# Kernel optimization log

Hardware: AMD Instinct MI355X
Metric: run time of the kernel (lower is better)

## Reference

```python
import jax, jax.numpy as jnp
import numpy as np

V, T, K, L, D = 256, 256, 36, 32, 1024
TAU = 0.05
MODE = 0
NEG_INF = -jnp.inf


def setup_inputs() -> dict:
    key = jax.random.key(0)
    k1, k2 = jax.random.split(key)
    imgs = jax.random.normal(k1, (V, K, D), dtype=jnp.float32)
    caps = jax.random.normal(k2, (T, L, D), dtype=jnp.float32)
    # Full lengths: the original module writes -inf into sim and 0 into w at
    # padded positions, so padding would produce -inf*0 = NaN in the output.
    img_lens = jnp.full((V,), K, dtype=jnp.int32)
    cap_lens = jnp.full((T,), L, dtype=jnp.int32)
    return {"imgs": imgs, "caps": caps, "img_lens": img_lens, "cap_lens": cap_lens}


def _l2norm(x):
    return x / jnp.maximum(jnp.linalg.norm(x, axis=-1, keepdims=True), 1e-12)


def reference(imgs, caps, img_lens, cap_lens):
    # masks: [V,K], [T,L]
    img_mask = (jnp.arange(K)[None, :] < img_lens[:, None]).astype(imgs.dtype)
    cap_mask = (jnp.arange(L)[None, :] < cap_lens[:, None]).astype(caps.dtype)
    # AvePool: masked mean over valid tokens, then L2-normalize
    img_glo = _l2norm((imgs * img_mask[:, :, None]).sum(1) / img_lens[:, None].astype(imgs.dtype))
    cap_glo = _l2norm((caps * cap_mask[:, :, None]).sum(1) / cap_lens[:, None].astype(caps.dtype))
    # ds: [V,T,K], et: [V,T,L]  (computed as in the original; note the original
    # forward overwrites w with the masked sim, so ds/et/softmax do not affect
    # the returned value — we keep only the live dataflow here)
    ds = jnp.einsum('vkd,td->vtk', imgs, cap_glo)
    et = jnp.einsum('tld,vd->vtl', caps, img_glo)
    del ds, et  # dead in the original (w is reassigned to masked sim)
    # sim: [V,T,K,L]
    sim = jnp.einsum('vkd,tld->vtkl', imgs, caps)
    sim_mask = img_mask[:, None, :, None] * cap_mask[None, :, None, :]  # [V,T,K,L]
    valid = sim_mask != 0
    sim = jnp.where(valid, sim, NEG_INF)
    # final w in the original is sim.masked_fill(sim_mask == 0, 0)
    w = jnp.where(valid, sim, 0.0)
    return jnp.einsum('vtkl,vtkl->vt', sim, w)
```

## Files before the change

kernel.cpp:

```cpp
#include <hip/hip_runtime.h>

#define V_N 256
#define T_N 256
#define K_N 36
#define L_N 32
#define D_N 1024
#define MROWS (V_N * K_N)
#define NROWS (T_N * L_N)
#define BM 256
#define BN 256
#define BK 64
#define KSTEPS (D_N / BK)
#define NBM (MROWS / BM)
#define NBN (NROWS / BN)
#define NWG (NBM * NBN)

typedef __attribute__((ext_vector_type(8))) short bf16x8;
typedef __attribute__((ext_vector_type(4))) float f32x4;

__device__ __forceinline__ ushort f2bf(float x) {
  union { float f; unsigned int u; } c; c.f = x;
  unsigned int r = c.u + 0x7FFFu + ((c.u >> 16) & 1u);
  return (ushort)(r >> 16);
}

__global__ void cvt_cast(const float* __restrict__ imgs, const float* __restrict__ caps,
                         ushort* __restrict__ aws, ushort* __restrict__ bws) {
  const int AQ = MROWS * (D_N / 4);
  const int BQ = NROWS * (D_N / 4);
  const int total = AQ + BQ;
  for (int q = blockIdx.x * blockDim.x + threadIdx.x; q < total;
       q += gridDim.x * blockDim.x) {
    float4 f;
    ushort4* dst;
    if (q < AQ) {
      f = reinterpret_cast<const float4*>(imgs)[q];
      dst = reinterpret_cast<ushort4*>(aws) + q;
    } else {
      f = reinterpret_cast<const float4*>(caps)[q - AQ];
      dst = reinterpret_cast<ushort4*>(bws) + (q - AQ);
    }
    ushort4 u; u.x = f2bf(f.x); u.y = f2bf(f.y); u.z = f2bf(f.z); u.w = f2bf(f.w);
    *dst = u;
  }
}

__global__ __launch_bounds__(512, 2) void gemm2(
    const ushort* __restrict__ aws, const ushort* __restrict__ bws,
    float* __restrict__ out) {
  __shared__ ushort lds[2 * 2 * BM * BK];

  int orig = (int)blockIdx.x;
  int wg = (orig & 7) * (NWG / 8) + (orig >> 3);
  const int bm = wg / NBN;
  const int bn = wg % NBN;
  const int row0 = bm * BM;
  const int col0 = bn * BN;

  const int tid  = (int)threadIdx.x;
  const int lane = tid & 63;
  const int wid  = tid >> 6;
  const int wr   = wid >> 2;
  const int wc   = wid & 3;

  auto stageA = [&](int kt) {
    ushort* bufA = lds + (kt & 1) * (2 * BM * BK);
#pragma unroll
    for (int it = 0; it < 4; ++it) {
      int q = it * 512 + tid;
      int r = q >> 3;
      int sw = ((q & 7) << 4) ^ ((r & 7) << 4);
      const ushort* ga = aws + (size_t)(row0 + r) * D_N + kt * BK + (sw >> 1);
      __builtin_amdgcn_global_load_lds(
          (const __attribute__((address_space(1))) void*)ga,
          (__attribute__((address_space(3))) void*)(bufA + q * 8), 16, 0, 0);
    }
  };
  auto stageB = [&](int kt) {
    ushort* bufB = lds + (kt & 1) * (2 * BM * BK) + BM * BK;
#pragma unroll
    for (int it = 0; it < 4; ++it) {
      int q = it * 512 + tid;
      int r = q >> 3;
      int sw = ((q & 7) << 4) ^ ((r & 7) << 4);
      const ushort* gb = bws + (size_t)(col0 + r) * D_N + kt * BK + (sw >> 1);
      __builtin_amdgcn_global_load_lds(
          (const __attribute__((address_space(1))) void*)gb,
          (__attribute__((address_space(3))) void*)(bufB + q * 8), 16, 0, 0);
    }
  };

  f32x4 acc[8][4];
#pragma unroll
  for (int m = 0; m < 8; ++m)
#pragma unroll
    for (int n = 0; n < 4; ++n) acc[m][n] = (f32x4){0.f, 0.f, 0.f, 0.f};

  const int arow = wr * 128 + (lane & 15);
  const int brow = wc * 64 + (lane & 15);
  const int kb   = (lane >> 4) << 4;
  const int swz  = (lane & 7) << 4;

  auto tile = [&](int t, int do_stage) {
    const ushort* bufA = lds + (t & 1) * (2 * BM * BK);
    const ushort* bufB = bufA + BM * BK;
    const int sw0 = (kb) ^ swz;
    const int sw1 = (64 + kb) ^ swz;

    bf16x8 a0[8], a1[8], b0[4], b1[4];
#pragma unroll
    for (int m = 0; m < 4; ++m)
      a0[m] = *reinterpret_cast<const bf16x8*>(bufA + (arow + m * 16) * BK + (sw0 >> 1));
#pragma unroll
    for (int n = 0; n < 4; ++n)
      b0[n] = *reinterpret_cast<const bf16x8*>(bufB + (brow + n * 16) * BK + (sw0 >> 1));
#pragma unroll
    for (int m = 4; m < 8; ++m)
      a0[m] = *reinterpret_cast<const bf16x8*>(bufA + (arow + m * 16) * BK + (sw0 >> 1));
#pragma unroll
    for (int m = 0; m < 4; ++m)
      a1[m] = *reinterpret_cast<const bf16x8*>(bufA + (arow + m * 16) * BK + (sw1 >> 1));
#pragma unroll
    for (int n = 0; n < 4; ++n)
      b1[n] = *reinterpret_cast<const bf16x8*>(bufB + (brow + n * 16) * BK + (sw1 >> 1));
#pragma unroll
    for (int m = 4; m < 8; ++m)
      a1[m] = *reinterpret_cast<const bf16x8*>(bufA + (arow + m * 16) * BK + (sw1 >> 1));

    __builtin_amdgcn_s_setprio(1);
#pragma unroll
    for (int m = 0; m < 4; ++m)
#pragma unroll
      for (int n = 0; n < 4; ++n)
        acc[m][n] = __builtin_amdgcn_mfma_f32_16x16x32_bf16(a0[m], b0[n], acc[m][n], 0, 0, 0);
    __builtin_amdgcn_s_setprio(0);
    __builtin_amdgcn_s_setprio(1);
#pragma unroll
    for (int m = 4; m < 8; ++m)
#pragma unroll
      for (int n = 0; n < 4; ++n)
        acc[m][n] = __builtin_amdgcn_mfma_f32_16x16x32_bf16(a0[m], b0[n], acc[m][n], 0, 0, 0);
    __builtin_amdgcn_s_setprio(0);
    __builtin_amdgcn_s_setprio(1);
#pragma unroll
    for (int m = 0; m < 4; ++m)
#pragma unroll
      for (int n = 0; n < 4; ++n)
        acc[m][n] = __builtin_amdgcn_mfma_f32_16x16x32_bf16(a1[m], b1[n], acc[m][n], 0, 0, 0);
    __builtin_amdgcn_s_setprio(0);

    asm volatile("s_waitcnt lgkmcnt(0)" ::: "memory");
    __builtin_amdgcn_sched_barrier(0);
    __builtin_amdgcn_s_barrier();
    __builtin_amdgcn_sched_barrier(0);

    if (do_stage) { stageA(t + 2); stageB(t + 2); }

    __builtin_amdgcn_s_setprio(1);
#pragma unroll
    for (int m = 4; m < 8; ++m)
#pragma unroll
      for (int n = 0; n < 4; ++n)
        acc[m][n] = __builtin_amdgcn_mfma_f32_16x16x32_bf16(a1[m], b1[n], acc[m][n], 0, 0, 0);
    __builtin_amdgcn_s_setprio(0);
  };

  stageA(0); stageB(0);
  stageA(1); stageB(1);
  asm volatile("s_waitcnt vmcnt(8)" ::: "memory");
  __builtin_amdgcn_sched_barrier(0);
  __builtin_amdgcn_s_barrier();
  __builtin_amdgcn_sched_barrier(0);

  for (int t = 0; t < KSTEPS - 2; ++t) {
    tile(t, 1);
    asm volatile("s_waitcnt vmcnt(8)" ::: "memory");
    __builtin_amdgcn_sched_barrier(0);
    __builtin_amdgcn_s_barrier();
    __builtin_amdgcn_sched_barrier(0);
  }
  tile(KSTEPS - 2, 0);
  asm volatile("s_waitcnt vmcnt(0)" ::: "memory");
  __builtin_amdgcn_sched_barrier(0);
  __builtin_amdgcn_s_barrier();
  __builtin_amdgcn_sched_barrier(0);
  tile(KSTEPS - 1, 0);

#pragma unroll
  for (int m = 0; m < 8; ++m) {
    int grow = row0 + wr * 128 + m * 16;
    int v0 = grow / K_N;
    int b = (v0 + 1) * K_N;
    int rb = grow + ((lane >> 4) << 2);
#pragma unroll
    for (int np = 0; np < 2; ++np) {
      float s0 = 0.f, s1 = 0.f;
#pragma unroll
      for (int nn = 0; nn < 2; ++nn) {
        f32x4 a4 = acc[m][np * 2 + nn];
#pragma unroll
        for (int rg = 0; rg < 4; ++rg) {
          float x = a4[rg];
          float x2 = x * x;
          if (rb + rg < b) s0 += x2; else s1 += x2;
        }
      }
#pragma unroll
      for (int off = 32; off > 0; off >>= 1) {
        s0 += __shfl_xor(s0, off, 64);
        s1 += __shfl_xor(s1, off, 64);
      }
      if (lane == 0) {
        int tcol = (col0 + wc * 64 + np * 32) >> 5;
        atomicAdd(out + v0 * T_N + tcol, s0);
        if (grow + 16 > b) atomicAdd(out + (v0 + 1) * T_N + tcol, s1);
      }
    }
  }
}

__global__ __launch_bounds__(256) void gemm_fb(
    const float* __restrict__ imgs, const float* __restrict__ caps,
    float* __restrict__ out) {
  __shared__ ushort lds[128 * 64 + 128 * 64];
  ushort* ldsA = lds;
  ushort* ldsB = lds + 128 * 64;
  const int NBMf = MROWS / 128, NBNf = NROWS / 128;
  int orig = (int)blockIdx.x;
  int xcd = orig & 7;
  int idx = orig >> 3;
  int bm = xcd * (NBMf / 8) + (idx / NBNf);
  int bn = idx % NBNf;
  const int row0 = bm * 128, col0 = bn * 128;
  const int tid = (int)threadIdx.x, lane = tid & 63, wid = tid >> 6;
  const int wr = wid >> 1, wc = wid & 1;
  f32x4 acc[4][4];
#pragma unroll
  for (int i = 0; i < 4; ++i)
#pragma unroll
    for (int j = 0; j < 4; ++j) acc[i][j] = (f32x4){0.f, 0.f, 0.f, 0.f};
  for (int kt = 0; kt < KSTEPS; ++kt) {
#pragma unroll
    for (int it = 0; it < 4; ++it) {
      int q = it * 256 + tid;
      int r = q >> 3;
      int sw = ((q & 7) << 4) ^ ((r & 7) << 4);
      const float4* src = reinterpret_cast<const float4*>(
          imgs + (size_t)(row0 + r) * D_N + kt * BK + (sw >> 1));
      float4 f0 = src[0], f1 = src[1];
      union { ushort u[8]; int4 v4; } pk;
      pk.u[0] = f2bf(f0.x); pk.u[1] = f2bf(f0.y); pk.u[2] = f2bf(f0.z); pk.u[3] = f2bf(f0.w);
      pk.u[4] = f2bf(f1.x); pk.u[5] = f2bf(f1.y); pk.u[6] = f2bf(f1.z); pk.u[7] = f2bf(f1.w);
      *reinterpret_cast<int4*>(ldsA + q * 8) = pk.v4;
    }
#pragma unroll
    for (int it = 0; it < 4; ++it) {
      int q = it * 256 + tid;
      int r = q >> 3;
      int sw = ((q & 7) << 4) ^ ((r & 7) << 4);
      const float4* src = reinterpret_cast<const float4*>(
          caps + (size_t)(col0 + r) * D_N + kt * BK + (sw >> 1));
      float4 f0 = src[0], f1 = src[1];
      union { ushort u[8]; int4 v4; } pk;
      pk.u[0] = f2bf(f0.x); pk.u[1] = f2bf(f0.y); pk.u[2] = f2bf(f0.z); pk.u[3] = f2bf(f0.w);
      pk.u[4] = f2bf(f1.x); pk.u[5] = f2bf(f1.y); pk.u[6] = f2bf(f1.z); pk.u[7] = f2bf(f1.w);
      *reinterpret_cast<int4*>(ldsB + q * 8) = pk.v4;
    }
    __syncthreads();
#pragma unroll
    for (int ks = 0; ks < 2; ++ks) {
      bf16x8 afr[4], bfr[4];
#pragma unroll
      for (int i = 0; i < 4; ++i) {
        int r = wr * 64 + i * 16 + (lane & 15);
        int sw = (ks * 64 + (((lane >> 4) << 4))) ^ ((r & 7) << 4);
        afr[i] = *reinterpret_cast<const bf16x8*>(ldsA + r * BK + (sw >> 1));
      }
#pragma unroll
      for (int j = 0; j < 4; ++j) {
        int r = wc * 64 + j * 16 + (lane & 15);
        int sw = (ks * 64 + (((lane >> 4) << 4))) ^ ((r & 7) << 4);
        bfr[j] = *reinterpret_cast<const bf16x8*>(ldsB + r * BK + (sw >> 1));
      }
#pragma unroll
      for (int i = 0; i < 4; ++i)
#pragma unroll
        for (int j = 0; j < 4; ++j)
          acc[i][j] = __builtin_amdgcn_mfma_f32_16x16x32_bf16(afr[i], bfr[j], acc[i][j], 0, 0, 0);
    }
    __syncthreads();
  }
#pragma unroll
  for (int i = 0; i < 4; ++i) {
#pragma unroll
    for (int j = 0; j < 4; ++j) {
      f32x4 a4 = acc[i][j];
      int grow = row0 + wr * 64 + i * 16;
      int gcol = col0 + wc * 64 + j * 16;
      int t = gcol >> 5;
      int v0 = grow / K_N;
      int b = (v0 + 1) * K_N;
      int rbase = grow + ((lane >> 4) << 2);
      float s0 = 0.f, s1 = 0.f;
#pragma unroll
      for (int rg = 0; rg < 4; ++rg) {
        float x = a4[rg];
        float x2 = x * x;
        if (rbase + rg < b) s0 += x2; else s1 += x2;
      }
#pragma unroll
      for (int off = 32; off > 0; off >>= 1) {
        s0 += __shfl_xor(s0, off, 64);
        s1 += __shfl_xor(s1, off, 64);
      }
      if (lane == 0) {
        atomicAdd(out + v0 * T_N + t, s0);
        if (b < grow + 16) atomicAdd(out + (v0 + 1) * T_N + t, s1);
      }
    }
  }
}

extern "C" void kernel_launch(void* const* d_in, const int* in_sizes, int n_in,
                              void* d_out, int out_size, void* d_ws, size_t ws_size,
                              hipStream_t stream) {
  const float* imgs = (const float*)d_in[0];
  const float* caps = (const float*)d_in[1];
  float* out = (float*)d_out;

  hipMemsetAsync(d_out, 0, (size_t)V_N * T_N * sizeof(float), stream);

  const size_t need = (size_t)(MROWS + NROWS) * D_N * sizeof(ushort);

  if (ws_size >= need) {
    ushort* aws = (ushort*)d_ws;
    ushort* bws = aws + (size_t)MROWS * D_N;
    cvt_cast<<<2048, 256, 0, stream>>>(imgs, caps, aws, bws);
    gemm2<<<NWG, 512, 0, stream>>>(aws, bws, out);
  } else {
    const int nwg = (MROWS / 128) * (NROWS / 128);
    gemm_fb<<<nwg, 256, 0, stream>>>(imgs, caps, out);
  }
}
```

Baseline: 197.8 us.

## Split GEMM main loop into four quadrant phases with staggered LDS staging

```diff
diff --git a/kernel.cpp b/kernel.cpp
--- a/kernel.cpp
+++ b/kernel.cpp
@@ -17,6 +17,10 @@
 
 typedef __attribute__((ext_vector_type(8))) short bf16x8;
 typedef __attribute__((ext_vector_type(4))) float f32x4;
+
+#define SB0 __builtin_amdgcn_sched_barrier(0)
+#define BAR __builtin_amdgcn_s_barrier()
+#define LGK0 asm volatile("s_waitcnt lgkmcnt(0)" ::: "memory")
 
 __device__ __forceinline__ ushort f2bf(float x) {
   union { float f; unsigned int u; } c; c.f = x;
@@ -63,32 +67,36 @@
   const int wr   = wid >> 2;
   const int wc   = wid & 3;
 
-  auto stageA = [&](int kt) {
-    ushort* bufA = lds + (kt & 1) * (2 * BM * BK);
-#pragma unroll
-    for (int it = 0; it < 4; ++it) {
-      int q = it * 512 + tid;
-      int r = q >> 3;
-      int sw = ((q & 7) << 4) ^ ((r & 7) << 4);
-      const ushort* ga = aws + (size_t)(row0 + r) * D_N + kt * BK + (sw >> 1);
+  const int kb  = (lane >> 4) << 4;
+
+  auto stage_unit = [&](int kt, int kind) {
+    const int rb0 = (kind == 0) ? 0 : (kind == 1) ? 64 : (kind == 2) ? 0 : 128;
+    const int rb1 = (kind == 0) ? 128 : (kind == 1) ? 192 : (kind == 2) ? 64 : 192;
+    ushort* base = lds + (kt & 1) * (2 * BM * BK) + ((kind >= 2) ? BM * BK : 0);
+    const ushort* g = (kind >= 2) ? bws : aws;
+    const int g0 = (kind >= 2) ? col0 : row0;
+#pragma unroll
+    for (int j = 0; j < 2; ++j) {
+      int r = (j ? rb1 : rb0) + (tid >> 3);
+      int sw = ((tid & 7) << 4) ^ ((r & 7) << 4);
+      const ushort* src = g + (size_t)(g0 + r) * D_N + kt * BK + (sw >> 1);
       __builtin_amdgcn_global_load_lds(
-          (const __attribute__((address_space(1))) void*)ga,
-          (__attribute__((address_space(3))) void*)(bufA + q * 8), 16, 0, 0);
+          (const __attribute__((address_space(1))) void*)src,
+          (__attribute__((address_space(3))) void*)(base + r * BK + (tid & 7) * 8),
+          16, 0, 0);
     }
   };
-  auto stageB = [&](int kt) {
-    ushort* bufB = lds + (kt & 1) * (2 * BM * BK) + BM * BK;
-#pragma unroll
-    for (int it = 0; it < 4; ++it) {
-      int q = it * 512 + tid;
-      int r = q >> 3;
-      int sw = ((q & 7) << 4) ^ ((r & 7) << 4);
-      const ushort* gb = bws + (size_t)(col0 + r) * D_N + kt * BK + (sw >> 1);
-      __builtin_amdgcn_global_load_lds(
-          (const __attribute__((address_space(1))) void*)gb,
-          (__attribute__((address_space(3))) void*)(bufB + q * 8), 16, 0, 0);
-    }
+
+  auto rdA = [&](const ushort* bufA, int m, int ks) -> bf16x8 {
+    int r = wr * 128 + m * 16 + (lane & 15);
+    int sw = (ks * 64 + kb) ^ ((r & 7) << 4);
+    return *reinterpret_cast<const bf16x8*>(bufA + r * BK + (sw >> 1));
   };
+  auto rdB = [&](const ushort* bufB, int n, int ks) -> bf16x8 {
+    int r = wc * 64 + n * 16 + (lane & 15);
+    int sw = (ks * 64 + kb) ^ ((r & 7) << 4);
+    return *reinterpret_cast<const bf16x8*>(bufB + r * BK + (sw >> 1));
+  };
 
   f32x4 acc[8][4];
 #pragma unroll
@@ -96,95 +104,94 @@
 #pragma unroll
     for (int n = 0; n < 4; ++n) acc[m][n] = (f32x4){0.f, 0.f, 0.f, 0.f};
 
-  const int arow = wr * 128 + (lane & 15);
-  const int brow = wc * 64 + (lane & 15);
-  const int kb   = (lane >> 4) << 4;
-  const int swz  = (lane & 7) << 4;
-
-  auto tile = [&](int t, int do_stage) {
+  stage_unit(0, 0); stage_unit(0, 2); stage_unit(0, 3); stage_unit(0, 1);
+  stage_unit(1, 0); stage_unit(1, 2); stage_unit(1, 3);
+  asm volatile("s_waitcnt vmcnt(6)" ::: "memory");
+  SB0; BAR; SB0;
+
+  for (int t = 0; t < KSTEPS; ++t) {
     const ushort* bufA = lds + (t & 1) * (2 * BM * BK);
     const ushort* bufB = bufA + BM * BK;
-    const int sw0 = (kb) ^ swz;
-    const int sw1 = (64 + kb) ^ swz;
-
-    bf16x8 a0[8], a1[8], b0[4], b1[4];
-#pragma unroll
-    for (int m = 0; m < 4; ++m)
-      a0[m] = *reinterpret_cast<const bf16x8*>(bufA + (arow + m * 16) * BK + (sw0 >> 1));
-#pragma unroll
-    for (int n = 0; n < 4; ++n)
-      b0[n] = *reinterpret_cast<const bf16x8*>(bufB + (brow + n * 16) * BK + (sw0 >> 1));
-#pragma unroll
-    for (int m = 4; m < 8; ++m)
-      a0[m] = *reinterpret_cast<const bf16x8*>(bufA + (arow + m * 16) * BK + (sw0 >> 1));
-#pragma unroll
-    for (int m = 0; m < 4; ++m)
-      a1[m] = *reinterpret_cast<const bf16x8*>(bufA + (arow + m * 16) * BK + (sw1 >> 1));
-#pragma unroll
-    for (int n = 0; n < 4; ++n)
-      b1[n] = *reinterpret_cast<const bf16x8*>(bufB + (brow + n * 16) * BK + (sw1 >> 1));
-#pragma unroll
-    for (int m = 4; m < 8; ++m)
-      a1[m] = *reinterpret_cast<const bf16x8*>(bufA + (arow + m * 16) * BK + (sw1 >> 1));
-
+    bf16x8 aA[8], b01[4], b23[4];
+
+#pragma unroll
+    for (int m = 0; m < 4; ++m) { aA[m] = rdA(bufA, m, 0); aA[4 + m] = rdA(bufA, m, 1); }
+#pragma unroll
+    for (int n = 0; n < 2; ++n) { b01[n] = rdB(bufB, n, 0); b01[2 + n] = rdB(bufB, n, 1); }
+    if (t <= KSTEPS - 2) stage_unit(t + 1, 1);
+    SB0; BAR; LGK0; SB0;
     __builtin_amdgcn_s_setprio(1);
 #pragma unroll
     for (int m = 0; m < 4; ++m)
 #pragma unroll
-      for (int n = 0; n < 4; ++n)
-        acc[m][n] = __builtin_amdgcn_mfma_f32_16x16x32_bf16(a0[m], b0[n], acc[m][n], 0, 0, 0);
+      for (int n = 0; n < 2; ++n)
+        acc[m][n] = __builtin_amdgcn_mfma_f32_16x16x32_bf16(aA[m], b01[n], acc[m][n], 0, 0, 0);
+#pragma unroll
+    for (int m = 0; m < 4; ++m)
+#pragma unroll
+      for (int n = 0; n < 2; ++n)
+        acc[m][n] = __builtin_amdgcn_mfma_f32_16x16x32_bf16(aA[4 + m], b01[2 + n], acc[m][n], 0, 0, 0);
     __builtin_amdgcn_s_setprio(0);
+    SB0; BAR;
+
+#pragma unroll
+    for (int n = 0; n < 2; ++n) { b23[n] = rdB(bufB, 2 + n, 0); b23[2 + n] = rdB(bufB, 2 + n, 1); }
+    if (t <= KSTEPS - 3) stage_unit(t + 2, 0);
+    SB0; BAR; LGK0; SB0;
     __builtin_amdgcn_s_setprio(1);
 #pragma unroll
-    for (int m = 4; m < 8; ++m)
-#pragma unroll
-      for (int n = 0; n < 4; ++n)
-        acc[m][n] = __builtin_amdgcn_mfma_f32_16x16x32_bf16(a0[m], b0[n], acc[m][n], 0, 0, 0);
+    for (int m = 0; m < 4; ++m)
+#pragma unroll
+      for (int n = 0; n < 2; ++n)
+        acc[m][2 + n] = __builtin_amdgcn_mfma_f32_16x16x32_bf16(aA[m], b23[n], acc[m][2 + n], 0, 0, 0);
+#pragma unroll
+    for (int m = 0; m < 4; ++m)
+#pragma unroll
+      for (int n = 0; n < 2; ++n)
+        acc[m][2 + n] = __builtin_amdgcn_mfma_f32_16x16x32_bf16(aA[4 + m], b23[2 + n], acc[m][2 + n], 0, 0, 0);
     __builtin_amdgcn_s_setprio(0);
+    if (t <= KSTEPS - 3)      { asm volatile("s_waitcnt vmcnt(10)" ::: "memory"); }
+    else if (t == KSTEPS - 2) { asm volatile("s_waitcnt vmcnt(8)"  ::: "memory"); }
+    else                      { asm volatile("s_waitcnt vmcnt(0)"  ::: "memory"); }
+    SB0; BAR;
+
+#pragma unroll
+    for (int m = 0; m < 4; ++m) { aA[m] = rdA(bufA, 4 + m, 0); aA[4 + m] = rdA(bufA, 4 + m, 1); }
+    if (t <= KSTEPS - 3) stage_unit(t + 2, 2);
+    SB0; BAR; LGK0; SB0;
     __builtin_amdgcn_s_setprio(1);
 #pragma unroll
     for (int m = 0; m < 4; ++m)
 #pragma unroll
-      for (int n = 0; n < 4; ++n)
-        acc[m][n] = __builtin_amdgcn_mfma_f32_16x16x32_bf16(a1[m], b1[n], acc[m][n], 0, 0, 0);
+      for (int n = 0; n < 2; ++n)
+        acc[4 + m][n] = __builtin_amdgcn_mfma_f32_16x16x32_bf16(aA[m], b01[n], acc[4 + m][n], 0, 0, 0);
+#pragma unroll
+    for (int m = 0; m < 4; ++m)
+#pragma unroll
+      for (int n = 0; n < 2; ++n)
+        acc[4 + m][n] = __builtin_amdgcn_mfma_f32_16x16x32_bf16(aA[4 + m], b01[2 + n], acc[4 + m][n], 0, 0, 0);
     __builtin_amdgcn_s_setprio(0);
-
-    asm volatile("s_waitcnt lgkmcnt(0)" ::: "memory");
-    __builtin_amdgcn_sched_barrier(0);
-    __builtin_amdgcn_s_barrier();
-    __builtin_amdgcn_sched_barrier(0);
-
-    if (do_stage) { stageA(t + 2); stageB(t + 2); }
-
+    SB0; BAR;
+
+    if (t <= KSTEPS - 3) stage_unit(t + 2, 3);
+    SB0; BAR;
     __builtin_amdgcn_s_setprio(1);
 #pragma unroll
-    for (int m = 4; m < 8; ++m)
-#pragma unroll
-      for (int n = 0; n < 4; ++n)
-        acc[m][n] = __builtin_amdgcn_mfma_f32_16x16x32_bf16(a1[m], b1[n], acc[m][n], 0, 0, 0);
+    for (int m = 0; m < 4; ++m)
+#pragma unroll
+      for (int n = 0; n < 2; ++n)
+        acc[4 + m][2 + n] = __builtin_amdgcn_mfma_f32_16x16x32_bf16(aA[m], b23[n], acc[4 + m][2 + n], 0, 0, 0);
+#pragma unroll
+    for (int m = 0; m < 4; ++m)
+#pragma unroll
+      for (int n = 0; n < 2; ++n)
+        acc[4 + m][2 + n] = __builtin_amdgcn_mfma_f32_16x16x32_bf16(aA[4 + m], b23[2 + n], acc[4 + m][2 + n], 0, 0, 0);
     __builtin_amdgcn_s_setprio(0);
-  };
-
-  stageA(0); stageB(0);
-  stageA(1); stageB(1);
-  asm volatile("s_waitcnt vmcnt(8)" ::: "memory");
-  __builtin_amdgcn_sched_barrier(0);
-  __builtin_amdgcn_s_barrier();
-  __builtin_amdgcn_sched_barrier(0);
-
-  for (int t = 0; t < KSTEPS - 2; ++t) {
-    tile(t, 1);
-    asm volatile("s_waitcnt vmcnt(8)" ::: "memory");
-    __builtin_amdgcn_sched_barrier(0);
-    __builtin_amdgcn_s_barrier();
-    __builtin_amdgcn_sched_barrier(0);
-  }
-  tile(KSTEPS - 2, 0);
-  asm volatile("s_waitcnt vmcnt(0)" ::: "memory");
-  __builtin_amdgcn_sched_barrier(0);
-  __builtin_amdgcn_s_barrier();
-  __builtin_amdgcn_sched_barrier(0);
-  tile(KSTEPS - 1, 0);
+    if (t <= KSTEPS - 3)      { asm volatile("s_waitcnt vmcnt(8)" ::: "memory"); }
+    else if (t == KSTEPS - 2) { asm volatile("s_waitcnt vmcnt(2)" ::: "memory"); }
+    else                      { asm volatile("s_waitcnt vmcnt(0)" ::: "memory"); }
+    SB0; BAR;
+  }
 
 #pragma unroll
   for (int m = 0; m < 8; ++m) {
```

New measurement: 196.4 us. About the same (-0.7%).
